# Optimization experiments

Hardware: AMD Instinct MI355X
Metric: run time of the kernel (lower is better)

Reference implementation:

```python
import jax, jax.numpy as jnp
import numpy as np

B, S, E = 4, 2048, 1024


def setup_inputs() -> dict:
    key = jax.random.key(0)
    ks = jax.random.split(key, 7)
    sc = 1.0 / np.sqrt(E)
    return {
        "embedded": jax.random.normal(ks[0], (B, S, E), dtype=jnp.float32),
        "Wk": jax.random.normal(ks[1], (E, E), dtype=jnp.float32) * sc,
        "bk": jax.random.normal(ks[2], (E,), dtype=jnp.float32) * 0.01,
        "Wq": jax.random.normal(ks[3], (E, E), dtype=jnp.float32) * sc,
        "bq": jax.random.normal(ks[4], (E,), dtype=jnp.float32) * 0.01,
        "Wv": jax.random.normal(ks[5], (E, E), dtype=jnp.float32) * sc,
        "bv": jax.random.normal(ks[6], (E,), dtype=jnp.float32) * 0.01,
    }


def reference(embedded, Wk, bk, Wq, bq, Wv, bv):
    # embedded: [B, S, E]
    K = embedded @ Wk.T + bk  # [B,S,E]
    Q = embedded @ Wq.T + bq
    V = embedded @ Wv.T + bv
    seq_len = K.shape[1]
    # score[b,i,j] = K_i . Q_j, scaled by 1/sqrt(seq_len) (as in original)
    scores = jnp.einsum('bie,bje->bij', K, Q) / jnp.sqrt(jnp.asarray(seq_len, K.dtype))
    # softmax over dim=-2 -> over the key index i
    W = jax.nn.softmax(scores, axis=-2)  # [B,S,S]
    # Y = (V^T @ W)^T -> Y[b,j,d] = sum_i V[b,i,d] * W[b,i,j]
    Y = jnp.einsum('bid,bij->bjd', V, W)  # [B,S,E]
    return Y
```

## Files before the change

### kernel.cpp

```cpp
#include <hip/hip_runtime.h>
#include <hip/hip_bf16.h>


typedef __bf16 bf16x8 __attribute__((ext_vector_type(8)));
typedef float  f32x4  __attribute__((ext_vector_type(4)));

__device__ __forceinline__ unsigned short f2bf(float f) {
    unsigned int u = __float_as_uint(f);
    u = (u + 0x7FFFu + ((u >> 16) & 1u)) >> 16;
    return (unsigned short)u;
}

__global__ __launch_bounds__(256)
void cvt_all(const float* __restrict__ X,  const float* __restrict__ Wq,
             const float* __restrict__ Wk, const float* __restrict__ Wv,
             unsigned short* __restrict__ Xb,  unsigned short* __restrict__ Wqb,
             unsigned short* __restrict__ Wkb, unsigned short* __restrict__ Wvb,
             float* __restrict__ l) {
    long i = (long)blockIdx.x * 256 + threadIdx.x;
    if (i < 8192) l[i] = 0.0f;
    const float* src; unsigned short* dst; long off;
    if (i < 2097152L) { src = X; dst = Xb; off = i; }
    else {
        long j = i - 2097152L;
        int w = (int)(j >> 18);
        off = j & 262143L;
        src = (w == 0) ? Wq : (w == 1) ? Wk : Wv;
        dst = (w == 0) ? Wqb : (w == 1) ? Wkb : Wvb;
    }
    float4 v = reinterpret_cast<const float4*>(src)[off];
    ushort4 o;
    o.x = f2bf(v.x); o.y = f2bf(v.y); o.z = f2bf(v.z); o.w = f2bf(v.w);
    reinterpret_cast<ushort4*>(dst)[off] = o;
}

#define GEMM_DECLS                                                      \
    const int t    = threadIdx.x;                                       \
    const int wave = t >> 6;                                            \
    const int lane = t & 63;                                            \
    const int quad = lane >> 4;                                         \
    const int lr   = lane & 15;                                         \
    const int wm   = (wave >> 1) * 64;                                  \
    const int wn   = (wave & 1) * 64;                                   \
    const int sx   = lr & 7;                                            \
    const int lrow = lane >> 3;                                         \
    const int gch  = ((lane & 7) ^ (lrow & 7)) * 8;

#define GEMM_KLOOP(Aptr, Bptr, LDA, LDB)                                \
    for (int k0 = 0; k0 < K; k0 += 64) {                                \
        _Pragma("unroll")                                               \
        for (int r = 0; r < 4; ++r) {                                   \
            const int rowb = wave * 8 + r * 32;                         \
            const int row  = rowb + lrow;                               \
            const long goffA = (long)(m0 + row) * (LDA) + k0 + gch;     \
            const long goffB = (long)(n0 + row) * (LDB) + k0 + gch;     \
            __builtin_amdgcn_global_load_lds(                           \
                (const __attribute__((address_space(1))) void*)((Aptr) + goffA), \
                (__attribute__((address_space(3))) void*)(&lsA[rowb * 64]), 16, 0, 0); \
            __builtin_amdgcn_global_load_lds(                           \
                (const __attribute__((address_space(1))) void*)((Bptr) + goffB), \
                (__attribute__((address_space(3))) void*)(&lsB[rowb * 64]), 16, 0, 0); \
        }                                                               \
        __syncthreads();                                                \
        _Pragma("unroll")                                               \
        for (int h = 0; h < 2; ++h) {                                   \
            const int cp = ((h * 4 + quad) ^ sx) * 8;                   \
            bf16x8 af[4], bfr[4];                                       \
            _Pragma("unroll")                                           \
            for (int i = 0; i < 4; ++i) {                               \
                af[i]  = __builtin_bit_cast(bf16x8,                     \
                          *reinterpret_cast<const uint4*>(&lsA[(wm + i * 16 + lr) * 64 + cp])); \
                bfr[i] = __builtin_bit_cast(bf16x8,                     \
                          *reinterpret_cast<const uint4*>(&lsB[(wn + i * 16 + lr) * 64 + cp])); \
            }                                                           \
            _Pragma("unroll")                                           \
            for (int i = 0; i < 4; ++i)                                 \
                _Pragma("unroll")                                       \
                for (int j = 0; j < 4; ++j)                             \
                    acc[i][j] = __builtin_amdgcn_mfma_f32_16x16x32_bf16(af[i], bfr[j], acc[i][j], 0, 0, 0); \
        }                                                               \
        __syncthreads();                                                \
    }

__global__ __launch_bounds__(256, 4)
void gemm_qkv(const unsigned short* __restrict__ Xb,
              const unsigned short* __restrict__ Wqb,
              const unsigned short* __restrict__ Wkb,
              const unsigned short* __restrict__ Wvb,
              const float* __restrict__ bq, const float* __restrict__ bk,
              const float* __restrict__ bv_,
              unsigned short* __restrict__ Qb, unsigned short* __restrict__ Kb,
              unsigned short* __restrict__ Vt)
{
    __shared__ unsigned short lsA[128 * 64];
    __shared__ unsigned short lsB[128 * 64];

    const int id  = blockIdx.x;
    const int g   = id & 7;
    const int jj  = id >> 3;
    const int xx  = jj & 7;
    const int yin = (jj >> 3) & 7;
    const int z   = jj >> 6;

    const unsigned short* A = Xb;
    const unsigned short* B = (z == 0) ? Wqb : (z == 1) ? Wkb : Wvb;
    const float* bias       = (z == 0) ? bq  : (z == 1) ? bk  : bv_;

    const int n0 = xx * 128;
    const int m0 = (g * 8 + yin) * 128;
    const int K = 1024;

    GEMM_DECLS
    f32x4 acc[4][4] = {};
    GEMM_KLOOP(A, B, 1024, 1024)

#pragma unroll
    for (int j = 0; j < 4; ++j) {
        const int n = n0 + wn + j * 16 + lr;
        const float bvv = bias[n];
#pragma unroll
        for (int i = 0; i < 4; ++i) {
            const int mbase = m0 + wm + i * 16 + quad * 4;
            if (z < 2) {
                unsigned short* C = (z == 0) ? Qb : Kb;
#pragma unroll
                for (int r = 0; r < 4; ++r)
                    C[(long)(mbase + r) * 1024 + n] = f2bf(acc[i][j][r] + bvv);
            } else {
                ushort4 o;
                o.x = f2bf(acc[i][j][0] + bvv);
                o.y = f2bf(acc[i][j][1] + bvv);
                o.z = f2bf(acc[i][j][2] + bvv);
                o.w = f2bf(acc[i][j][3] + bvv);
                long boff = (long)(mbase >> 11) * (1024L * 2048) + (long)n * 2048 + (mbase & 2047);
                *reinterpret_cast<ushort4*>(Vt + boff) = o;
            }
        }
    }
}

__global__ __launch_bounds__(256, 4)
void gemm_scores(const unsigned short* __restrict__ Q,
                 const unsigned short* __restrict__ Kp,
                 unsigned short* __restrict__ P, float* __restrict__ l,
                 float scale)
{
    __shared__ unsigned short lsA[128 * 64];
    __shared__ unsigned short lsB[128 * 64];

    const int id  = blockIdx.x;
    const int g   = id & 7;
    const int u   = id >> 3;
    const int bz  = g >> 1;
    const int mh  = g & 1;
    const int yin = u & 7;
    const int xx  = u >> 3;

    const unsigned short* A = Q  + (long)bz * 2048 * 1024;
    const unsigned short* B = Kp + (long)bz * 2048 * 1024;
    unsigned short* Pb = P + (long)bz * 2048 * 2048;
    float* lb = l + bz * 2048;

    const int n0 = xx * 128;
    const int m0 = (mh * 8 + yin) * 128;
    const int K = 1024;

    GEMM_DECLS
    f32x4 acc[4][4] = {};
    GEMM_KLOOP(A, B, 1024, 1024)

#pragma unroll
    for (int i = 0; i < 4; ++i) {
#pragma unroll
        for (int r = 0; r < 4; ++r) {
            const int m = m0 + wm + i * 16 + quad * 4 + r;
            float psum = 0.0f;
#pragma unroll
            for (int j = 0; j < 4; ++j) {
                const float p = __expf(acc[i][j][r] * scale);
                psum += p;
                const int n = n0 + wn + j * 16 + lr;
                Pb[(long)m * 2048 + n] = f2bf(p);
            }
#pragma unroll
            for (int o = 1; o < 16; o <<= 1) psum += __shfl_xor(psum, o, 64);
            if (lr == 0) atomicAdd(&lb[m], psum);
        }
    }
}

__global__ __launch_bounds__(256, 4)
void gemm_y(const unsigned short* __restrict__ P,
            const unsigned short* __restrict__ Vt,
            const float* __restrict__ l, float* __restrict__ out)
{
    __shared__ unsigned short lsA[128 * 64];
    __shared__ unsigned short lsB[128 * 64];

    const int id  = blockIdx.x;
    const int g   = id & 7;
    const int u   = id >> 3;
    const int bz  = g >> 1;
    const int mh  = g & 1;
    const int yin = u & 7;
    const int xx  = u >> 3;

    const unsigned short* A = P  + (long)bz * 2048 * 2048;
    const unsigned short* B = Vt + (long)bz * 1024 * 2048;
    const float* lb = l + bz * 2048;
    float* C = out + (long)bz * 2048 * 1024;

    const int n0 = xx * 128;
    const int m0 = (mh * 8 + yin) * 128;
    const int K = 2048;

    GEMM_DECLS
    f32x4 acc[4][4] = {};
    GEMM_KLOOP(A, B, 2048, 2048)

    float linv[4][4];
#pragma unroll
    for (int i = 0; i < 4; ++i)
#pragma unroll
        for (int r = 0; r < 4; ++r)
            linv[i][r] = 1.0f / lb[m0 + wm + i * 16 + quad * 4 + r];

#pragma unroll
    for (int j = 0; j < 4; ++j) {
        const int n = n0 + wn + j * 16 + lr;
#pragma unroll
        for (int i = 0; i < 4; ++i) {
            const int mbase = m0 + wm + i * 16 + quad * 4;
#pragma unroll
            for (int r = 0; r < 4; ++r)
                C[(long)(mbase + r) * 1024 + n] = acc[i][j][r] * linv[i][r];
        }
    }
}

extern "C" void kernel_launch(void* const* d_in, const int* in_sizes, int n_in,
                              void* d_out, int out_size, void* d_ws, size_t ws_size,
                              hipStream_t stream) {
    const float* X  = (const float*)d_in[0];
    const float* Wk = (const float*)d_in[1];
    const float* bk = (const float*)d_in[2];
    const float* Wq = (const float*)d_in[3];
    const float* bq = (const float*)d_in[4];
    const float* Wv = (const float*)d_in[5];
    const float* bv = (const float*)d_in[6];
    float* out = (float*)d_out;

    const size_t MB = 1024 * 1024;
    if (ws_size < 80 * MB) return;

    char* ws = (char*)d_ws;
    unsigned short* Vt  = (unsigned short*)(ws);
    unsigned short* P   = (unsigned short*)(ws + 16 * MB);
    unsigned short* Xbf = (unsigned short*)(ws + 16 * MB);
    float*          l   = (float*)(ws + 48 * MB);
    unsigned short* Wqb = (unsigned short*)(ws + 49 * MB);
    unsigned short* Wkb = (unsigned short*)(ws + 51 * MB);
    unsigned short* Wvb = (unsigned short*)(ws + 53 * MB);
    unsigned short* Qb = (unsigned short*)d_out;
    unsigned short* Kb = Qb + 8192L * 1024;

    dim3 blk(256);

    cvt_all<<<2883584 / 256, blk, 0, stream>>>(X, Wq, Wk, Wv, Xbf, Wqb, Wkb, Wvb, l);

    gemm_qkv<<<1536, blk, 0, stream>>>(Xbf, Wqb, Wkb, Wvb, bq, bk, bv, Qb, Kb, Vt);

    gemm_scores<<<1024, blk, 0, stream>>>(Qb, Kb, P, l, 0.022097086912079608f);

    gemm_y<<<512, blk, 0, stream>>>(P, Vt, l, out);
}
```

Before: 231.8 us.

## Fuse four kernel launches into one cooperative persistent kernel with grid syncs

```diff
diff --git a/kernel.cpp b/kernel.cpp
--- a/kernel.cpp
+++ b/kernel.cpp
@@ -1,5 +1,8 @@
 #include <hip/hip_runtime.h>
 #include <hip/hip_bf16.h>
+#include <hip/hip_cooperative_groups.h>
+
+namespace cg = cooperative_groups;
 
 
 typedef __bf16 bf16x8 __attribute__((ext_vector_type(8)));
@@ -9,29 +12,6 @@
     unsigned int u = __float_as_uint(f);
     u = (u + 0x7FFFu + ((u >> 16) & 1u)) >> 16;
     return (unsigned short)u;
-}
-
-__global__ __launch_bounds__(256)
-void cvt_all(const float* __restrict__ X,  const float* __restrict__ Wq,
-             const float* __restrict__ Wk, const float* __restrict__ Wv,
-             unsigned short* __restrict__ Xb,  unsigned short* __restrict__ Wqb,
-             unsigned short* __restrict__ Wkb, unsigned short* __restrict__ Wvb,
-             float* __restrict__ l) {
-    long i = (long)blockIdx.x * 256 + threadIdx.x;
-    if (i < 8192) l[i] = 0.0f;
-    const float* src; unsigned short* dst; long off;
-    if (i < 2097152L) { src = X; dst = Xb; off = i; }
-    else {
-        long j = i - 2097152L;
-        int w = (int)(j >> 18);
-        off = j & 262143L;
-        src = (w == 0) ? Wq : (w == 1) ? Wk : Wv;
-        dst = (w == 0) ? Wqb : (w == 1) ? Wkb : Wvb;
-    }
-    float4 v = reinterpret_cast<const float4*>(src)[off];
-    ushort4 o;
-    o.x = f2bf(v.x); o.y = f2bf(v.y); o.z = f2bf(v.z); o.w = f2bf(v.w);
-    reinterpret_cast<ushort4*>(dst)[off] = o;
 }
 
 #define GEMM_DECLS                                                      \
@@ -82,27 +62,46 @@
         __syncthreads();                                                \
     }
 
-__global__ __launch_bounds__(256, 4)
-void gemm_qkv(const unsigned short* __restrict__ Xb,
-              const unsigned short* __restrict__ Wqb,
-              const unsigned short* __restrict__ Wkb,
-              const unsigned short* __restrict__ Wvb,
-              const float* __restrict__ bq, const float* __restrict__ bk,
-              const float* __restrict__ bv_,
-              unsigned short* __restrict__ Qb, unsigned short* __restrict__ Kb,
-              unsigned short* __restrict__ Vt)
-{
-    __shared__ unsigned short lsA[128 * 64];
-    __shared__ unsigned short lsB[128 * 64];
-
-    const int id  = blockIdx.x;
-    const int g   = id & 7;
-    const int jj  = id >> 3;
+
+__device__ __forceinline__ void cvt_step(
+    long i, const float* __restrict__ X, const float* __restrict__ Wq,
+    const float* __restrict__ Wk, const float* __restrict__ Wv,
+    unsigned short* __restrict__ Xb, unsigned short* __restrict__ Wqb,
+    unsigned short* __restrict__ Wkb, unsigned short* __restrict__ Wvb,
+    float* __restrict__ l)
+{
+    if (i < 8192) l[i] = 0.0f;
+    const float* src; unsigned short* dst; long off;
+    if (i < 2097152L) { src = X; dst = Xb; off = i; }
+    else {
+        long j = i - 2097152L;
+        int w = (int)(j >> 18);
+        off = j & 262143L;
+        src = (w == 0) ? Wq : (w == 1) ? Wk : Wv;
+        dst = (w == 0) ? Wqb : (w == 1) ? Wkb : Wvb;
+    }
+    float4 v = reinterpret_cast<const float4*>(src)[off];
+    ushort4 o;
+    o.x = f2bf(v.x); o.y = f2bf(v.y); o.z = f2bf(v.z); o.w = f2bf(v.w);
+    reinterpret_cast<ushort4*>(dst)[off] = o;
+}
+
+__device__ __forceinline__ void qkv_tile(
+    int tt, unsigned short* lsA, unsigned short* lsB,
+    const unsigned short* __restrict__ Xb,
+    const unsigned short* __restrict__ Wqb, const unsigned short* __restrict__ Wkb,
+    const unsigned short* __restrict__ Wvb,
+    const float* __restrict__ bq, const float* __restrict__ bk,
+    const float* __restrict__ bv_,
+    unsigned short* __restrict__ Qb, unsigned short* __restrict__ Kb,
+    unsigned short* __restrict__ Vt)
+{
+    const int g   = tt & 7;
+    const int jj  = tt >> 3;
     const int xx  = jj & 7;
     const int yin = (jj >> 3) & 7;
     const int z   = jj >> 6;
 
-    const unsigned short* A = Xb;
     const unsigned short* B = (z == 0) ? Wqb : (z == 1) ? Wkb : Wvb;
     const float* bias       = (z == 0) ? bq  : (z == 1) ? bk  : bv_;
 
@@ -112,7 +111,7 @@
 
     GEMM_DECLS
     f32x4 acc[4][4] = {};
-    GEMM_KLOOP(A, B, 1024, 1024)
+    GEMM_KLOOP(Xb, B, 1024, 1024)
 
 #pragma unroll
     for (int j = 0; j < 4; ++j) {
@@ -139,22 +138,18 @@
     }
 }
 
-__global__ __launch_bounds__(256, 4)
-void gemm_scores(const unsigned short* __restrict__ Q,
-                 const unsigned short* __restrict__ Kp,
-                 unsigned short* __restrict__ P, float* __restrict__ l,
-                 float scale)
-{
-    __shared__ unsigned short lsA[128 * 64];
-    __shared__ unsigned short lsB[128 * 64];
-
-    const int id  = blockIdx.x;
+__device__ __forceinline__ void scores_tile(
+    int id, unsigned short* lsA, unsigned short* lsB,
+    const unsigned short* __restrict__ Q, const unsigned short* __restrict__ Kp,
+    unsigned short* __restrict__ P, float* __restrict__ l)
+{
+    const float scale = 0.022097086912079608f;
     const int g   = id & 7;
-    const int u   = id >> 3;
+    const int uu  = id >> 3;
     const int bz  = g >> 1;
     const int mh  = g & 1;
-    const int yin = u & 7;
-    const int xx  = u >> 3;
+    const int yin = uu & 7;
+    const int xx  = uu >> 3;
 
     const unsigned short* A = Q  + (long)bz * 2048 * 1024;
     const unsigned short* B = Kp + (long)bz * 2048 * 1024;
@@ -189,21 +184,17 @@
     }
 }
 
-__global__ __launch_bounds__(256, 4)
-void gemm_y(const unsigned short* __restrict__ P,
-            const unsigned short* __restrict__ Vt,
-            const float* __restrict__ l, float* __restrict__ out)
-{
-    __shared__ unsigned short lsA[128 * 64];
-    __shared__ unsigned short lsB[128 * 64];
-
-    const int id  = blockIdx.x;
+__device__ __forceinline__ void y_tile(
+    int id, unsigned short* lsA, unsigned short* lsB,
+    const unsigned short* __restrict__ P, const unsigned short* __restrict__ Vt,
+    const float* __restrict__ l, float* __restrict__ out)
+{
     const int g   = id & 7;
-    const int u   = id >> 3;
+    const int uu  = id >> 3;
     const int bz  = g >> 1;
     const int mh  = g & 1;
-    const int yin = u & 7;
-    const int xx  = u >> 3;
+    const int yin = uu & 7;
+    const int xx  = uu >> 3;
 
     const unsigned short* A = P  + (long)bz * 2048 * 2048;
     const unsigned short* B = Vt + (long)bz * 1024 * 2048;
@@ -236,6 +227,79 @@
                 C[(long)(mbase + r) * 1024 + n] = acc[i][j][r] * linv[i][r];
         }
     }
+}
+
+__global__ __launch_bounds__(256, 4)
+void fused_attn(const float* __restrict__ X,  const float* __restrict__ Wq,
+                const float* __restrict__ Wk, const float* __restrict__ Wv,
+                const float* __restrict__ bq, const float* __restrict__ bk,
+                const float* __restrict__ bv_,
+                unsigned short* __restrict__ Xb,
+                unsigned short* __restrict__ Wqb, unsigned short* __restrict__ Wkb,
+                unsigned short* __restrict__ Wvb,
+                unsigned short* __restrict__ Qb, unsigned short* __restrict__ Kb,
+                unsigned short* __restrict__ Vt, unsigned short* __restrict__ P,
+                float* __restrict__ l, float* __restrict__ out)
+{
+    __shared__ unsigned short lsA[128 * 64];
+    __shared__ unsigned short lsB[128 * 64];
+    cg::grid_group grid = cg::this_grid();
+    const int bid = blockIdx.x;
+
+    for (int vb = bid; vb < 11264; vb += 1024)
+        cvt_step((long)vb * 256 + threadIdx.x, X, Wq, Wk, Wv, Xb, Wqb, Wkb, Wvb, l);
+    grid.sync();
+
+    for (int tt = bid; tt < 1536; tt += 1024)
+        qkv_tile(tt, lsA, lsB, Xb, Wqb, Wkb, Wvb, bq, bk, bv_, Qb, Kb, Vt);
+    grid.sync();
+
+    scores_tile(bid, lsA, lsB, Qb, Kb, P, l);
+    grid.sync();
+
+    if (bid < 512)
+        y_tile(bid, lsA, lsB, P, Vt, l, out);
+}
+
+__global__ __launch_bounds__(256)
+void cvt_all(const float* __restrict__ X,  const float* __restrict__ Wq,
+             const float* __restrict__ Wk, const float* __restrict__ Wv,
+             unsigned short* __restrict__ Xb,  unsigned short* __restrict__ Wqb,
+             unsigned short* __restrict__ Wkb, unsigned short* __restrict__ Wvb,
+             float* __restrict__ l) {
+    cvt_step((long)blockIdx.x * 256 + threadIdx.x, X, Wq, Wk, Wv, Xb, Wqb, Wkb, Wvb, l);
+}
+
+__global__ __launch_bounds__(256, 4)
+void gemm_qkv(const unsigned short* __restrict__ Xb,
+              const unsigned short* __restrict__ Wqb,
+              const unsigned short* __restrict__ Wkb,
+              const unsigned short* __restrict__ Wvb,
+              const float* __restrict__ bq, const float* __restrict__ bk,
+              const float* __restrict__ bv_,
+              unsigned short* __restrict__ Qb, unsigned short* __restrict__ Kb,
+              unsigned short* __restrict__ Vt) {
+    __shared__ unsigned short lsA[128 * 64];
+    __shared__ unsigned short lsB[128 * 64];
+    qkv_tile(blockIdx.x, lsA, lsB, Xb, Wqb, Wkb, Wvb, bq, bk, bv_, Qb, Kb, Vt);
+}
+
+__global__ __launch_bounds__(256, 4)
+void gemm_scores(const unsigned short* __restrict__ Q,
+                 const unsigned short* __restrict__ Kp,
+                 unsigned short* __restrict__ P, float* __restrict__ l) {
+    __shared__ unsigned short lsA[128 * 64];
+    __shared__ unsigned short lsB[128 * 64];
+    scores_tile(blockIdx.x, lsA, lsB, Q, Kp, P, l);
+}
+
+__global__ __launch_bounds__(256, 4)
+void gemm_y(const unsigned short* __restrict__ P,
+            const unsigned short* __restrict__ Vt,
+            const float* __restrict__ l, float* __restrict__ out) {
+    __shared__ unsigned short lsA[128 * 64];
+    __shared__ unsigned short lsB[128 * 64];
+    y_tile(blockIdx.x, lsA, lsB, P, Vt, l, out);
 }
 
 extern "C" void kernel_launch(void* const* d_in, const int* in_sizes, int n_in,
@@ -264,13 +328,20 @@
     unsigned short* Qb = (unsigned short*)d_out;
     unsigned short* Kb = Qb + 8192L * 1024;
 
-    dim3 blk(256);
-
-    cvt_all<<<2883584 / 256, blk, 0, stream>>>(X, Wq, Wk, Wv, Xbf, Wqb, Wkb, Wvb, l);
-
-    gemm_qkv<<<1536, blk, 0, stream>>>(Xbf, Wqb, Wkb, Wvb, bq, bk, bv, Qb, Kb, Vt);
-
-    gemm_scores<<<1024, blk, 0, stream>>>(Qb, Kb, P, l, 0.022097086912079608f);
-
-    gemm_y<<<512, blk, 0, stream>>>(P, Vt, l, out);
-}
+    void* args[] = { (void*)&X, (void*)&Wq, (void*)&Wk, (void*)&Wv,
+                     (void*)&bq, (void*)&bk, (void*)&bv,
+                     (void*)&Xbf, (void*)&Wqb, (void*)&Wkb, (void*)&Wvb,
+                     (void*)&Qb, (void*)&Kb, (void*)&Vt, (void*)&P,
+                     (void*)&l, (void*)&out };
+
+    hipError_t e = hipLaunchCooperativeKernel((const void*)fused_attn,
+                                              dim3(1024), dim3(256),
+                                              args, 0u, stream);
+    if (e != hipSuccess) {
+        dim3 blk(256);
+        cvt_all<<<11264, blk, 0, stream>>>(X, Wq, Wk, Wv, Xbf, Wqb, Wkb, Wvb, l);
+        gemm_qkv<<<1536, blk, 0, stream>>>(Xbf, Wqb, Wkb, Wvb, bq, bk, bv, Qb, Kb, Vt);
+        gemm_scores<<<1024, blk, 0, stream>>>(Qb, Kb, P, l);
+        gemm_y<<<512, blk, 0, stream>>>(P, Vt, l, out);
+    }
+}
```

Measured after the change: 623.4 us. +168.9%, slower.
